# Optimization experiments

Measured on AMD Instinct MI355X. Metric: run time of the kernel, lower is better.

Reference implementation:

```python
import jax, jax.numpy as jnp
import numpy as np

LRELU = 0.2
BN_EPS = 1e-5
SN_EPS = 1e-12


def _spectral_norm(w, u):
    # One power iteration (torch train-mode behavior), u/v detached.
    wm = w.reshape(w.shape[0], -1)            # [out, in*kh*kw]
    u = jax.lax.stop_gradient(u)
    v = wm.T @ u
    v = v / (jnp.linalg.norm(v) + SN_EPS)
    u2 = wm @ v
    u2 = u2 / (jnp.linalg.norm(u2) + SN_EPS)
    sigma = u2 @ (wm @ v)
    return w / sigma


def _conv(x, w):
    # Conv2d kernel=4, stride=2, padding=1, no bias
    return jax.lax.conv_general_dilated(
        x, w, window_strides=(2, 2), padding=((1, 1), (1, 1)),
        dimension_numbers=("NCHW", "OIHW", "NCHW"))


def _bn(x, g, b):
    # BatchNorm2d in training mode: biased batch stats over (N,H,W)
    m = x.mean(axis=(0, 2, 3), keepdims=True)
    v = x.var(axis=(0, 2, 3), keepdims=True)
    xh = (x - m) * jax.lax.rsqrt(v + BN_EPS)
    return xh * g[None, :, None, None] + b[None, :, None, None]


def _lrelu(x):
    return jnp.where(x >= 0, x, LRELU * x)


def setup_inputs() -> dict:
    key = jax.random.key(0)
    ks = jax.random.split(key, 16)
    ndf, nc, oc, N = 64, 3, 64, 64
    chans = [(nc, ndf), (ndf, ndf * 2), (ndf * 2, ndf * 4),
             (ndf * 4, ndf * 4), (ndf * 4, ndf * 8), (ndf * 8, oc)]
    inp = {"image": jax.random.normal(ks[0], (N, nc, 128, 128), jnp.float32)}
    for i, (ci, co) in enumerate(chans):
        inp[f"w{i+1}"] = 0.02 * jax.random.normal(ks[1 + i], (co, ci, 4, 4), jnp.float32)
        inp[f"u{i+1}"] = jax.random.normal(ks[7 + i], (co,), jnp.float32)
    for i, c in enumerate([ndf * 2, ndf * 4, ndf * 4, ndf * 8]):
        inp[f"g{i+1}"] = jnp.ones((c,), jnp.float32)
        inp[f"b{i+1}"] = jnp.zeros((c,), jnp.float32)
    A, B, C = oc * 2 * 2, oc, ndf  # 256, 64, 64
    stddev = 1.0 / A
    inp["T"] = jax.random.uniform(ks[13], (A, B, C), jnp.float32,
                                  minval=stddev, maxval=1.0)
    return inp


def reference(image, w1, w2, w3, w4, w5, w6, u1, u2, u3, u4, u5, u6,
              g1, b1, g2, b2, g3, b3, g4, b4, T):
    x = _lrelu(_conv(image, _spectral_norm(w1, u1)))
    x = _lrelu(_bn(_conv(x, _spectral_norm(w2, u2)), g1, b1))
    x = _lrelu(_bn(_conv(x, _spectral_norm(w3, u3)), g2, b2))
    x = _lrelu(_bn(_conv(x, _spectral_norm(w4, u4)), g3, b3))
    x = _lrelu(_bn(_conv(x, _spectral_norm(w5, u5)), g4, b4))
    x = _conv(x, _spectral_norm(w6, u6))          # [N, 64, 2, 2]; Dropout2d(p=0) = identity
    A, Bo, C = T.shape
    flat = x.reshape(-1, A)                        # [N, 256]
    Ms = (flat @ T.reshape(A, Bo * C)).reshape(-1, Bo, C)   # [N, B, C]
    # MiniBatchDiscrimination: out[i,b] = sum_j exp(-||Ms[i,b]-Ms[j,b]||_1)
    d = jnp.abs(Ms[:, None, :, :] - Ms[None, :, :, :]).sum(-1)  # [N, N, B]
    mbd = jnp.exp(-d).sum(axis=1)                  # [N, B]
    return jnp.concatenate([flat, mbd], axis=1)    # [N, 320]
```

## Files before the change

### kernel.cpp

```cpp
#include <hip/hip_runtime.h>
#include <hip/hip_bf16.h>
#include <math.h>

#define LRELU 0.2f
#define BN_EPS 1e-5f
#define SN_EPS 1e-12f

typedef __attribute__((ext_vector_type(4))) float f32x4;
typedef __attribute__((ext_vector_type(8))) short bf16x8;
typedef __attribute__((ext_vector_type(4))) short bf16x4;

__device__ inline float bf2f(short s) {
  union { unsigned u; float f; } c; c.u = ((unsigned)(unsigned short)s) << 16; return c.f;
}
__device__ inline short f2bf(float f) {
  __hip_bfloat16 h = __float2bfloat16(f); return *(short*)&h;
}

__device__ inline int xcd_swz(int bx, int nwg) {
  int chunk = nwg >> 3;
  return (bx & 7) * chunk + (bx >> 3);
}

__device__ inline float blockReduceSum256(float v, volatile float* red) {
  #pragma unroll
  for (int o = 32; o > 0; o >>= 1) v += __shfl_down(v, o, 64);
  const int tid = threadIdx.x;
  __syncthreads();
  if ((tid & 63) == 0) red[tid >> 6] = v;
  __syncthreads();
  return red[0] + red[1] + red[2] + red[3];
}

struct SNArgs {
  const float* w[6];
  const float* u[6];
  int outc[6];
  int ink[6];
};

__global__ __launch_bounds__(256) void sn_v(SNArgs args, float* __restrict__ vpart) {
  const int l = blockIdx.z;
  const int in_k = args.ink[l], out_c = args.outc[l];
  const int tid = threadIdx.x;
  const int j = blockIdx.x * 256 + tid;
  if (blockIdx.x * 256 >= in_k) return;
  const int rows = out_c >> 3;
  const int i0 = blockIdx.y * rows;
  __shared__ float uS[64];
  if (tid < rows) uS[tid] = args.u[l][i0 + tid];
  __syncthreads();
  if (j >= in_k) return;
  const float* __restrict__ w = args.w[l] + (size_t)i0 * in_k;
  float t = 0.f;
  for (int i = 0; i < rows; ++i) t = fmaf(w[(size_t)i * in_k + j], uS[i], t);
  vpart[((size_t)(l * 8 + blockIdx.y)) * 8192 + j] = t;
}

__global__ __launch_bounds__(256) void sn_v_red(SNArgs args, const float* __restrict__ vpart,
                                                float* __restrict__ vbuf, float* __restrict__ pA) {
  const int l = blockIdx.y;
  const int in_k = args.ink[l];
  const int tid = threadIdx.x;
  const int j = blockIdx.x * 256 + tid;
  __shared__ float red[4];
  float s = 0.f;
  if (j < in_k) {
    #pragma unroll
    for (int ch = 0; ch < 8; ++ch)
      s += vpart[((size_t)(l * 8 + ch)) * 8192 + j];
    vbuf[l * 8192 + j] = s;
  }
  const float bs = blockReduceSum256((j < in_k) ? s * s : 0.f, red);
  if (tid == 0) pA[l * 32 + blockIdx.x] = bs;
}

__global__ __launch_bounds__(64) void sn_norm1(SNArgs args, const float* __restrict__ pA,
                                               float* __restrict__ rinv) {
  const int l = blockIdx.x;
  if (threadIdx.x != 0) return;
  const int nb = (args.ink[l] + 255) >> 8;
  float s = 0.f;
  for (int b = 0; b < nb; ++b) s += pA[l * 32 + b];
  rinv[l] = 1.f / (sqrtf(s) + SN_EPS);
}

__global__ __launch_bounds__(256) void sn_t2(SNArgs args, const float* __restrict__ vbuf,
                                             const float* __restrict__ rinv,
                                             float* __restrict__ pB) {
  const int l = blockIdx.y;
  const int in_k = args.ink[l], out_c = args.outc[l];
  const int lane = threadIdx.x & 63, wv = threadIdx.x >> 6;
  const int row = blockIdx.x * 4 + wv;
  __shared__ float red[4];
  float sq = 0.f;
  if (row < out_c) {
    const float* __restrict__ wr = args.w[l] + (size_t)row * in_k;
    const float* __restrict__ v = vbuf + l * 8192;
    float a0 = 0.f, a1 = 0.f, a2 = 0.f, a3 = 0.f;
    for (int j = lane * 4; j < in_k; j += 256) {
      f32x4 w4 = *(const f32x4*)(wr + j);
      f32x4 v4 = *(const f32x4*)(v + j);
      a0 = fmaf(w4[0], v4[0], a0);
      a1 = fmaf(w4[1], v4[1], a1);
      a2 = fmaf(w4[2], v4[2], a2);
      a3 = fmaf(w4[3], v4[3], a3);
    }
    float t = (a0 + a1) + (a2 + a3);
    #pragma unroll
    for (int o = 32; o > 0; o >>= 1) t += __shfl_down(t, o, 64);
    if (lane == 0) { t *= rinv[l]; sq = t * t; }
  }
  __syncthreads();
  if (lane == 0) red[wv] = sq;
  __syncthreads();
  if (threadIdx.x == 0) pB[l * 128 + blockIdx.x] = red[0] + red[1] + red[2] + red[3];
}

__global__ __launch_bounds__(64) void sn_norm2(const float* __restrict__ pB,
                                               float* __restrict__ inv_sigma) {
  const int l = blockIdx.x;
  if (threadIdx.x != 0) return;
  float s = 0.f;
  for (int b = 0; b < 128; ++b) s += pB[l * 128 + b];
  const float n2 = sqrtf(s);
  const float sigma = s / (n2 + SN_EPS);
  inv_sigma[l] = 1.f / sigma;
}

__global__ __launch_bounds__(256) void zero_pads(__hip_bfloat16* r0, __hip_bfloat16* r1) {
  int t = blockIdx.x * 256 + threadIdx.x;
  if (t < 2048) {
    r0[16777216 + t] = __float2bfloat16(0.f);
    r1[16777216 + t] = __float2bfloat16(0.f);
  }
}

struct PPArgs {
  const float* w[6];
  __hip_bfloat16* dst[6];
  int cinr[6];
  int cout[6];
  int kpad[6];
  int kreal[6];
};

__global__ __launch_bounds__(256) void prepack_all(PPArgs args, const float* __restrict__ invs) {
  const int l = blockIdx.y;
  int e = blockIdx.x * 256 + threadIdx.x;
  const int total = args.kpad[l] * args.cout[l];
  if (e >= total) return;
  const int CINR = args.cinr[l], COUT = args.cout[l], KREAL = args.kreal[l];
  int j = e & 7, lane = (e >> 3) & 63, frag = e >> 9;
  int nfrags = COUT >> 4;
  int ks = frag / nfrags, nf = frag - ks * nfrags;
  int k = ks * 32 + ((lane >> 4) << 3) + j;
  int co = (nf << 4) + (lane & 15);
  float val = 0.f;
  if (k < KREAL) {
    int khw = k / CINR, ci = k - khw * CINR;
    int kh = khw >> 2, kw = khw & 3;
    val = args.w[l][(((size_t)co * CINR + ci) * 4 + kh) * 4 + kw] * invs[l];
  }
  args.dst[l][e] = __float2bfloat16(val);
}

__global__ __launch_bounds__(256) void im2col_l1(const float* __restrict__ img,
                                                 __hip_bfloat16* __restrict__ a2) {
  int t = blockIdx.x * 256 + threadIdx.x;
  int c = t & 7;
  int m = t >> 3;
  int n = m >> 12;
  int hw = m & 4095;
  int ho = hw >> 6, wo = hw & 63;
  int ihb = 2 * ho - 1, iwb = 2 * wo - 1;
  const float* __restrict__ ib = img + (size_t)n * 49152;
  short vals[8];
  #pragma unroll
  for (int j = 0; j < 8; ++j) {
    int k = c * 8 + j;
    float val = 0.f;
    if (k < 48) {
      int khw = k / 3;
      int ci = k - khw * 3;
      int kh = khw >> 2, kw = khw & 3;
      int ih = ihb + kh, iw = iwb + kw;
      if (((unsigned)ih < 128u) & ((unsigned)iw < 128u))
        val = ib[ci * 16384 + ih * 128 + iw];
    }
    vals[j] = f2bf(val);
  }
  *(bf16x8*)(a2 + (size_t)m * 64 + c * 8) = *(bf16x8*)vals;
}

template<int CIN, int COUT, int MF, bool FUSE>
__global__ __launch_bounds__(256) void conv_mfma(
    const __hip_bfloat16* __restrict__ x,
    const __hip_bfloat16* __restrict__ wf,
    __hip_bfloat16* __restrict__ out)
{
  constexpr int CB = CIN / 32;

  const int bx = xcd_swz(blockIdx.x, gridDim.x);
  const int lane = threadIdx.x & 63;
  const int wid  = threadIdx.x >> 6;
  const int wm = wid >> 1, wn = wid & 1;
  const int mbase = bx * (MF * 32) + wm * (MF * 16);
  const int cobase = blockIdx.y * 64 + wn * 32;

  int offm[MF];
  #pragma unroll
  for (int mf = 0; mf < MF; ++mf) {
    int m = mbase + mf * 16 + (lane & 15);
    offm[mf] = m * CIN;
  }
  const int koff = (lane >> 4) << 3;
  const __hip_bfloat16* wfp = wf + ((size_t)((blockIdx.y * 4 + wn * 2) * 64 + lane)) * 8;

  f32x4 acc[MF][2];
  #pragma unroll
  for (int mf = 0; mf < MF; ++mf) {
    acc[mf][0] = (f32x4){0.f, 0.f, 0.f, 0.f};
    acc[mf][1] = (f32x4){0.f, 0.f, 0.f, 0.f};
  }

  #pragma unroll
  for (int cb = 0; cb < CB; ++cb) {
    bf16x8 a[MF], b[2];
    #pragma unroll
    for (int mf = 0; mf < MF; ++mf) a[mf] = *(const bf16x8*)(x + offm[mf] + koff + cb * 32);
    #pragma unroll
    for (int nf = 0; nf < 2; ++nf)
      b[nf] = *(const bf16x8*)(wfp + (size_t)cb * (COUT * 32) + nf * 512);
    #pragma unroll
    for (int mf = 0; mf < MF; ++mf)
      #pragma unroll
      for (int nf = 0; nf < 2; ++nf)
        acc[mf][nf] = __builtin_amdgcn_mfma_f32_16x16x32_bf16(a[mf], b[nf], acc[mf][nf], 0, 0, 0);
  }

  const int r0 = (lane >> 4) * 4;
  const int cw = cobase + (lane & 15);
  #pragma unroll
  for (int mf = 0; mf < MF; ++mf)
    #pragma unroll
    for (int nf = 0; nf < 2; ++nf)
      #pragma unroll
      for (int r = 0; r < 4; ++r) {
        float v = acc[mf][nf][r];
        if (FUSE) v = (v >= 0.f) ? v : LRELU * v;
        int m = mbase + mf * 16 + r0 + r;
        out[(size_t)m * COUT + (cw + nf * 16)] = __float2bfloat16(v);
      }
}

template<int CIN, int COUT, int HIN, int HOUT, int Z, bool SPLITK, bool BNIN>
__global__ __launch_bounds__(256) void conv_lds(
    const __hip_bfloat16* __restrict__ x,
    const __hip_bfloat16* __restrict__ wf,
    const float* __restrict__ sbp,
    __hip_bfloat16* __restrict__ outb)
{
  constexpr int WIN = HIN, WO = HOUT;
  constexpr int CB = CIN / 32;
  constexpr int KHW_PER = 16 / Z;
  constexpr int NSTEP = KHW_PER * CB;
  constexpr int PADOFF = 16777216;
  constexpr int M = 64 * HOUT * WO;

  __shared__ __hip_bfloat16 As[128 * 32];
  __shared__ __hip_bfloat16 Bs[4096];

  const int bx = xcd_swz(blockIdx.x, gridDim.x);
  const int t = threadIdx.x;
  const int lane = t & 63;
  const int wid = t >> 6;
  const int wm = wid >> 1, wn = wid & 1;
  const int mbase = bx * 128;
  const int nbase = blockIdx.y * 128;
  const int khw0 = blockIdx.z * KHW_PER;

  const int sr0 = t >> 2;
  const int sl  = t & 3;
  const int wchunk = sl ^ ((sr0 >> 1) & 3);
  int rowbase[2], ihbs[2], iwbs[2];
  #pragma unroll
  for (int i = 0; i < 2; ++i) {
    int m = mbase + sr0 + i * 64;
    int n = m / (HOUT * WO);
    int hw = m - n * (HOUT * WO);
    int ho = hw / WO, wo = hw - ho * WO;
    ihbs[i] = 2 * ho - 1;
    iwbs[i] = 2 * wo - 1;
    rowbase[i] = ((n * HIN + ihbs[i]) * WIN + iwbs[i]) * CIN;
  }
  const size_t bslab0 = (size_t)(nbase >> 4) * 512 + (size_t)t * 8;

  f32x4 acc[4][4];
  #pragma unroll
  for (int mf = 0; mf < 4; ++mf)
    #pragma unroll
    for (int nf = 0; nf < 4; ++nf) acc[mf][nf] = (f32x4){0.f, 0.f, 0.f, 0.f};

  bf16x8 ra0, ra1, rb0, rb1;
  f32x4 sc0, sc1, of0, of1;
  bool v0 = true, v1 = true;
  auto load_step = [&](int ks) {
    const int khw = khw0 + ks / CB;
    const int cb = ks % CB;
    const int kh = khw >> 2, kw = khw & 3;
    const int kbyteoff = cb * 32 + sl * 8;
    {
      int ih = ihbs[0] + kh, iw = iwbs[0] + kw;
      v0 = ((unsigned)ih < (unsigned)HIN) & ((unsigned)iw < (unsigned)WIN);
      int off = v0 ? (rowbase[0] + (kh * WIN + kw) * CIN + kbyteoff) : PADOFF;
      ra0 = *(const bf16x8*)(x + off);
    }
    {
      int ih = ihbs[1] + kh, iw = iwbs[1] + kw;
      v1 = ((unsigned)ih < (unsigned)HIN) & ((unsigned)iw < (unsigned)WIN);
      int off = v1 ? (rowbase[1] + (kh * WIN + kw) * CIN + kbyteoff) : PADOFF;
      ra1 = *(const bf16x8*)(x + off);
    }
    const size_t kg = (size_t)khw * CB + cb;
    const size_t bo = kg * (COUT * 32) + bslab0;
    rb0 = *(const bf16x8*)(wf + bo);
    rb1 = *(const bf16x8*)(wf + bo + 2048);
    if (BNIN) {
      const int cbv = cb * 32 + sl * 8;
      sc0 = *(const f32x4*)(sbp + cbv);
      sc1 = *(const f32x4*)(sbp + cbv + 4);
      of0 = *(const f32x4*)(sbp + CIN + cbv);
      of1 = *(const f32x4*)(sbp + CIN + cbv + 4);
    }
  };

  load_step(0);
  for (int ks = 0; ks < NSTEP; ++ks) {
    __syncthreads();
    bf16x8 wa0 = ra0, wa1 = ra1;
    if (BNIN) {
      #pragma unroll
      for (int j = 0; j < 8; ++j) {
        float sc = (j < 4) ? sc0[j] : sc1[j - 4];
        float of = (j < 4) ? of0[j] : of1[j - 4];
        float f0 = fmaf(bf2f(wa0[j]), sc, of);
        f0 = fmaxf(f0, LRELU * f0);
        wa0[j] = v0 ? f2bf(f0) : (short)0;
        float f1 = fmaf(bf2f(wa1[j]), sc, of);
        f1 = fmaxf(f1, LRELU * f1);
        wa1[j] = v1 ? f2bf(f1) : (short)0;
      }
    }
    *(bf16x8*)(&As[sr0 * 32 + wchunk * 8]) = wa0;
    *(bf16x8*)(&As[(sr0 + 64) * 32 + wchunk * 8]) = wa1;
    *(bf16x8*)(&Bs[t * 8]) = rb0;
    *(bf16x8*)(&Bs[2048 + t * 8]) = rb1;
    __syncthreads();
    if (ks + 1 < NSTEP) load_step(ks + 1);
    bf16x8 af[4], bfr[4];
    #pragma unroll
    for (int mf = 0; mf < 4; ++mf) {
      const int ra = wm * 64 + mf * 16 + (lane & 15);
      const int rc = (lane >> 4) ^ ((ra >> 1) & 3);
      af[mf] = *(const bf16x8*)(&As[ra * 32 + rc * 8]);
    }
    #pragma unroll
    for (int nf = 0; nf < 4; ++nf)
      bfr[nf] = *(const bf16x8*)(&Bs[(wn * 4 + nf) * 512 + lane * 8]);
    #pragma unroll
    for (int mf = 0; mf < 4; ++mf)
      #pragma unroll
      for (int nf = 0; nf < 4; ++nf)
        acc[mf][nf] = __builtin_amdgcn_mfma_f32_16x16x32_bf16(af[mf], bfr[nf], acc[mf][nf], 0, 0, 0);
  }

  const int r0w = (lane >> 4) * 4;
  const int cw = nbase + wn * 64 + (lane & 15);
  #pragma unroll
  for (int mf = 0; mf < 4; ++mf)
    #pragma unroll
    for (int nf = 0; nf < 4; ++nf)
      #pragma unroll
      for (int r = 0; r < 4; ++r) {
        const int m = mbase + wm * 64 + mf * 16 + r0w + r;
        const int co = cw + nf * 16;
        if (SPLITK)
          outb[(size_t)blockIdx.z * M * COUT + (size_t)m * COUT + co] = __float2bfloat16(acc[mf][nf][r]);
        else
          outb[(size_t)m * COUT + co] = __float2bfloat16(acc[mf][nf][r]);
      }
}

template<int CIN, int COUT, int HIN, int HOUT, int Z, bool SPLITK, bool BNIN, bool BF16P>
__global__ __launch_bounds__(256) void conv_mfma4(
    const __hip_bfloat16* __restrict__ x,
    const __hip_bfloat16* __restrict__ wf,
    const float* __restrict__ sbp,
    __hip_bfloat16* __restrict__ outb, float* __restrict__ outp)
{
  constexpr int WIN = HIN, WO = HOUT;
  constexpr int CB = CIN / 32;
  constexpr int KHW_PER = 16 / Z;
  constexpr int PADOFF = 16777216;
  constexpr int M = 64 * HOUT * WO;

  const int bx = xcd_swz(blockIdx.x, gridDim.x);
  const int lane = threadIdx.x & 63;
  const int wid  = threadIdx.x >> 6;
  const int wm = wid >> 1, wn = wid & 1;
  const int mbase = bx * 128 + wm * 64;
  const int nbase = blockIdx.y * 128 + wn * 64;
  const int khw0 = blockIdx.z * KHW_PER;

  int offm[4], ihb[4], iwb[4];
  #pragma unroll
  for (int mf = 0; mf < 4; ++mf) {
    int m = mbase + mf * 16 + (lane & 15);
    int n = m / (HOUT * WO);
    int hw = m - n * (HOUT * WO);
    int ho = hw / WO, wo = hw - ho * WO;
    ihb[mf] = 2 * ho - 1;
    iwb[mf] = 2 * wo - 1;
    offm[mf] = ((n * HIN + ihb[mf]) * WIN + iwb[mf]) * CIN;
  }
  const int koff = (lane >> 4) << 3;
  const __hip_bfloat16* wfp = wf + ((size_t)((nbase >> 4) * 64 + lane)) * 8;

  f32x4 acc[4][4];
  #pragma unroll
  for (int mf = 0; mf < 4; ++mf)
    #pragma unroll
    for (int nf = 0; nf < 4; ++nf) acc[mf][nf] = (f32x4){0.f, 0.f, 0.f, 0.f};

  #pragma unroll
  for (int cb = 0; cb < CB; ++cb) {
    f32x4 s0, s1, o0, o1;
    if (BNIN) {
      const int cbase = cb * 32 + koff;
      s0 = *(const f32x4*)(sbp + cbase);
      s1 = *(const f32x4*)(sbp + cbase + 4);
      o0 = *(const f32x4*)(sbp + CIN + cbase);
      o1 = *(const f32x4*)(sbp + CIN + cbase + 4);
    }
    #pragma unroll
    for (int ki = 0; ki < KHW_PER; ++ki) {
      const int khw = khw0 + ki;
      const int kh = khw >> 2, kw = khw & 3;
      bf16x8 a[4], b[4];
      bool vm[4];
      #pragma unroll
      for (int mf = 0; mf < 4; ++mf) {
        int ih = ihb[mf] + kh, iw = iwb[mf] + kw;
        vm[mf] = ((unsigned)ih < (unsigned)HIN) & ((unsigned)iw < (unsigned)WIN);
        int off = vm[mf] ? (offm[mf] + (kh * WIN + kw) * CIN + koff + cb * 32)
                         : (PADOFF + koff + cb * 32);
        a[mf] = *(const bf16x8*)(x + off);
      }
      const size_t ks = (size_t)khw * CB + cb;
      #pragma unroll
      for (int nf = 0; nf < 4; ++nf)
        b[nf] = *(const bf16x8*)(wfp + ks * (COUT * 32) + nf * 512);
      if (BNIN) {
        #pragma unroll
        for (int mf = 0; mf < 4; ++mf) {
          bf16x8 tt = a[mf];
          #pragma unroll
          for (int j = 0; j < 8; ++j) {
            float fv = bf2f(tt[j]);
            float sc = (j < 4) ? s0[j] : s1[j - 4];
            float of = (j < 4) ? o0[j] : o1[j - 4];
            fv = fmaf(fv, sc, of);
            fv = fmaxf(fv, LRELU * fv);
            tt[j] = vm[mf] ? f2bf(fv) : (short)0;
          }
          a[mf] = tt;
        }
      }
      #pragma unroll
      for (int mf = 0; mf < 4; ++mf)
        #pragma unroll
        for (int nf = 0; nf < 4; ++nf)
          acc[mf][nf] = __builtin_amdgcn_mfma_f32_16x16x32_bf16(a[mf], b[nf], acc[mf][nf], 0, 0, 0);
    }
  }

  const int r0 = (lane >> 4) * 4;
  const int cw = nbase + (lane & 15);
  #pragma unroll
  for (int mf = 0; mf < 4; ++mf)
    #pragma unroll
    for (int nf = 0; nf < 4; ++nf)
      #pragma unroll
      for (int r = 0; r < 4; ++r) {
        const int m = mbase + mf * 16 + r0 + r;
        const int co = cw + nf * 16;
        if (SPLITK) {
          if (BF16P)
            outb[(size_t)blockIdx.z * M * COUT + (size_t)m * COUT + co] = __float2bfloat16(acc[mf][nf][r]);
          else
            outp[(size_t)blockIdx.z * M * COUT + (size_t)m * COUT + co] = acc[mf][nf][r];
        } else {
          outb[(size_t)m * COUT + co] = __float2bfloat16(acc[mf][nf][r]);
        }
      }
}

template<int Z, int MCHUNKS, bool BF16P>
__global__ __launch_bounds__(256) void sk_bn_fuse(const float* __restrict__ partf,
                                                  const __hip_bfloat16* __restrict__ partb,
                                                  __hip_bfloat16* __restrict__ xo,
                                                  float* __restrict__ statp, int M, int C) {
  const int chunk = blockIdx.x;
  const int c0 = blockIdx.y * 64 + (threadIdx.x & 7) * 8;
  const int mrow = threadIdx.x >> 3;
  const int rows = M / MCHUNKS;
  const size_t MC = (size_t)M * C;
  float s[8], s2[8];
  #pragma unroll
  for (int j = 0; j < 8; ++j) { s[j] = 0.f; s2[j] = 0.f; }
  for (int mi = mrow; mi < rows; mi += 32) {
    const int m = chunk * rows + mi;
    const size_t base = (size_t)m * C + c0;
    float av[8];
    if (BF16P) {
      bf16x8 v0 = *(const bf16x8*)(partb + base);
      #pragma unroll
      for (int j = 0; j < 8; ++j) av[j] = bf2f(v0[j]);
      #pragma unroll
      for (int z = 1; z < Z; ++z) {
        bf16x8 vz = *(const bf16x8*)(partb + (size_t)z * MC + base);
        #pragma unroll
        for (int j = 0; j < 8; ++j) av[j] += bf2f(vz[j]);
      }
    } else {
      f32x4 a = *(const f32x4*)(partf + base);
      f32x4 b = *(const f32x4*)(partf + base + 4);
      #pragma unroll
      for (int z = 1; z < Z; ++z) {
        a += *(const f32x4*)(partf + (size_t)z * MC + base);
        b += *(const f32x4*)(partf + (size_t)z * MC + base + 4);
      }
      #pragma unroll
      for (int j = 0; j < 4; ++j) { av[j] = a[j]; av[4 + j] = b[j]; }
    }
    bf16x8 o;
    #pragma unroll
    for (int j = 0; j < 8; ++j) {
      o[j] = f2bf(av[j]);
      s[j] += av[j];
      s2[j] = fmaf(av[j], av[j], s2[j]);
    }
    *(bf16x8*)(xo + base) = o;
  }
  __shared__ float ls[8][256], ls2[8][256];
  const int t = threadIdx.x;
  #pragma unroll
  for (int j = 0; j < 8; ++j) { ls[j][t] = s[j]; ls2[j][t] = s2[j]; }
  __syncthreads();
  #pragma unroll
  for (int off = 16; off >= 1; off >>= 1) {
    if (mrow < off) {
      #pragma unroll
      for (int j = 0; j < 8; ++j) {
        ls[j][t]  += ls[j][t + off * 8];
        ls2[j][t] += ls2[j][t + off * 8];
      }
    }
    __syncthreads();
  }
  if (t < 8) {
    #pragma unroll
    for (int j = 0; j < 8; ++j) {
      statp[(size_t)chunk * C + c0 + j] = ls[j][t];
      statp[(size_t)(MCHUNKS + chunk) * C + c0 + j] = ls2[j][t];
    }
  }
}

__global__ __launch_bounds__(256) void conv_l6_mfma(
    const __hip_bfloat16* __restrict__ x,
    const __hip_bfloat16* __restrict__ wf,
    float* __restrict__ x6, float* __restrict__ out)
{
  constexpr int CIN = 512, COUT = 64, HIN = 4;
  constexpr int CB = CIN / 32;
  constexpr int PADOFF = 16777216;

  const int lane = threadIdx.x & 63;
  const int wid  = threadIdx.x >> 6;
  const int wm = wid >> 1, wn = wid & 1;
  const int mbase = blockIdx.x * 32 + wm * 16;

  int m0 = mbase + (lane & 15);
  int n = m0 >> 2;
  int hw = m0 & 3;
  int ho = hw >> 1, wo = hw & 1;
  int ihb = 2 * ho - 1;
  int iwb = 2 * wo - 1;
  int offm = ((n * HIN + ihb) * HIN + iwb) * CIN;

  const int koff = (lane >> 4) << 3;
  const __hip_bfloat16* wfp = wf + ((size_t)((wn * 2) * 64 + lane)) * 8;

  f32x4 acc[2];
  acc[0] = (f32x4){0.f, 0.f, 0.f, 0.f};
  acc[1] = (f32x4){0.f, 0.f, 0.f, 0.f};

  #pragma unroll
  for (int khw = 0; khw < 16; ++khw) {
    const int kh = khw >> 2, kw = khw & 3;
    const int ih = ihb + kh, iw = iwb + kw;
    const bool v = ((unsigned)ih < (unsigned)HIN) & ((unsigned)iw < (unsigned)HIN);
    const int off = v ? (offm + (kh * HIN + kw) * CIN + koff) : (PADOFF + koff);
    const __hip_bfloat16* ap = x + off;
    #pragma unroll
    for (int cb = 0; cb < CB; ++cb) {
      const int ks = khw * CB + cb;
      bf16x8 a = *(const bf16x8*)(ap + cb * 32);
      bf16x8 b0 = *(const bf16x8*)(wfp + (size_t)ks * (COUT * 32));
      bf16x8 b1 = *(const bf16x8*)(wfp + (size_t)ks * (COUT * 32) + 512);
      acc[0] = __builtin_amdgcn_mfma_f32_16x16x32_bf16(a, b0, acc[0], 0, 0, 0);
      acc[1] = __builtin_amdgcn_mfma_f32_16x16x32_bf16(a, b1, acc[1], 0, 0, 0);
    }
  }

  const int r0 = (lane >> 4) * 4;
  const int cw = wn * 32 + (lane & 15);
  #pragma unroll
  for (int nf = 0; nf < 2; ++nf)
    #pragma unroll
    for (int r = 0; r < 4; ++r) {
      int m = mbase + r0 + r;
      int nn = m >> 2, p = m & 3;
      float v = acc[nf][r];
      x6[(size_t)nn * 256 + (cw + nf * 16) * 4 + p] = v;
      out[(size_t)nn * 320 + (cw + nf * 16) * 4 + p] = v;
    }
}

template<int MCHUNKS>
__global__ __launch_bounds__(256) void bn_stats_a(const __hip_bfloat16* __restrict__ x,
                                                  float* __restrict__ part, int M, int C) {
  const int chunk = blockIdx.x;
  const int c0 = blockIdx.y * 64 + (threadIdx.x & 7) * 8;
  const int mrow = threadIdx.x >> 3;
  const int rows = M / MCHUNKS;
  float s[8], s2[8];
  #pragma unroll
  for (int j = 0; j < 8; ++j) { s[j] = 0.f; s2[j] = 0.f; }
  for (int mi = mrow; mi < rows; mi += 32) {
    const int m = chunk * rows + mi;
    bf16x8 v = *(const bf16x8*)(x + (size_t)m * C + c0);
    #pragma unroll
    for (int j = 0; j < 8; ++j) {
      float f = bf2f(v[j]);
      s[j] += f;
      s2[j] = fmaf(f, f, s2[j]);
    }
  }
  __shared__ float ls[8][256], ls2[8][256];
  const int t = threadIdx.x;
  #pragma unroll
  for (int j = 0; j < 8; ++j) { ls[j][t] = s[j]; ls2[j][t] = s2[j]; }
  __syncthreads();
  #pragma unroll
  for (int off = 16; off >= 1; off >>= 1) {
    if (mrow < off) {
      #pragma unroll
      for (int j = 0; j < 8; ++j) {
        ls[j][t]  += ls[j][t + off * 8];
        ls2[j][t] += ls2[j][t + off * 8];
      }
    }
    __syncthreads();
  }
  if (t < 8) {
    #pragma unroll
    for (int j = 0; j < 8; ++j) {
      part[(size_t)chunk * C + c0 + j] = ls[j][t];
      part[(size_t)(MCHUNKS + chunk) * C + c0 + j] = ls2[j][t];
    }
  }
}

template<int MCHUNKS>
__global__ __launch_bounds__(64) void bn_stats_b(const float* __restrict__ part,
                                                 const float* __restrict__ g,
                                                 const float* __restrict__ b,
                                                 float* __restrict__ sb, int M, int C) {
  int c = blockIdx.x * 64 + threadIdx.x;
  float s = 0.f, s2 = 0.f;
  for (int ch = 0; ch < MCHUNKS; ++ch) {
    s  += part[(size_t)ch * C + c];
    s2 += part[(size_t)(MCHUNKS + ch) * C + c];
  }
  float invM = 1.f / (float)M;
  float mean = s * invM;
  float var = s2 * invM - mean * mean;
  float scale = g[c] * rsqrtf(var + BN_EPS);
  sb[c] = scale;
  sb[C + c] = b[c] - mean * scale;
}

__global__ __launch_bounds__(256) void bn_apply(__hip_bfloat16* __restrict__ x,
                                                const float* __restrict__ sb,
                                                int C, int nvec) {
  int idx = blockIdx.x * 256 + threadIdx.x;
  if (idx >= nvec) return;
  size_t e = (size_t)idx * 8;
  int c0 = (int)(e % (size_t)C);
  bf16x8 v = *(bf16x8*)(x + e);
  bf16x8 o;
  #pragma unroll
  for (int j = 0; j < 8; ++j) {
    int c = c0 + j;
    float f = bf2f(v[j]);
    f = fmaf(f, sb[c], sb[C + c]);
    f = (f >= 0.f) ? f : LRELU * f;
    o[j] = f2bf(f);
  }
  *(bf16x8*)(x + e) = o;
}

__global__ __launch_bounds__(256) void ms_kernel(const float* __restrict__ x6,
                                                 const float* __restrict__ T,
                                                 float* __restrict__ Ms) {
  const int cb = blockIdx.x;
  const int nb = blockIdx.y;
  const int c  = threadIdx.x & 63;
  const int ns = threadIdx.x >> 6;
  __shared__ float fsh[16][256];
  for (int t = threadIdx.x; t < 4096; t += 256) {
    int n = t >> 8, a = t & 255;
    fsh[n][a] = x6[(size_t)(nb * 16 + n) * 256 + a];
  }
  __syncthreads();
  const int col = cb * 64 + c;
  float acc0 = 0.f, acc1 = 0.f, acc2 = 0.f, acc3 = 0.f;
  #pragma unroll 8
  for (int a = 0; a < 256; ++a) {
    float tv = T[(size_t)a * 4096 + col];
    acc0 = fmaf(fsh[ns * 4 + 0][a], tv, acc0);
    acc1 = fmaf(fsh[ns * 4 + 1][a], tv, acc1);
    acc2 = fmaf(fsh[ns * 4 + 2][a], tv, acc2);
    acc3 = fmaf(fsh[ns * 4 + 3][a], tv, acc3);
  }
  const int nbase = nb * 16 + ns * 4;
  Ms[(size_t)(nbase + 0) * 4096 + col] = acc0;
  Ms[(size_t)(nbase + 1) * 4096 + col] = acc1;
  Ms[(size_t)(nbase + 2) * 4096 + col] = acc2;
  Ms[(size_t)(nbase + 3) * 4096 + col] = acc3;
}

__global__ __launch_bounds__(256) void mbd_kernel(const float* __restrict__ Ms,
                                                  float* __restrict__ out) {
  const int b  = blockIdx.x;
  const int ib = blockIdx.y;
  const int tid = threadIdx.x;
  __shared__ float Mb[64][65];
  for (int idx = tid; idx < 4096; idx += 256) {
    const int i = idx >> 6, cc = idx & 63;
    Mb[i][cc] = Ms[(size_t)i * 4096 + b * 64 + cc];
  }
  __syncthreads();
  const int i  = ib * 16 + (tid >> 4);
  const int jg = tid & 15;
  float ssum = 0.f;
  for (int j = jg; j < 64; j += 16) {
    float d = 0.f;
    #pragma unroll
    for (int cc = 0; cc < 64; ++cc) d += fabsf(Mb[i][cc] - Mb[j][cc]);
    ssum += expf(-d);
  }
  ssum += __shfl_xor(ssum, 1, 64);
  ssum += __shfl_xor(ssum, 2, 64);
  ssum += __shfl_xor(ssum, 4, 64);
  ssum += __shfl_xor(ssum, 8, 64);
  if (jg == 0) out[(size_t)i * 320 + 256 + b] = ssum;
}

extern "C" void kernel_launch(void* const* d_in, const int* in_sizes, int n_in,
                              void* d_out, int out_size, void* d_ws, size_t ws_size,
                              hipStream_t stream) {
  const float* image = (const float*)d_in[0];
  const float* W[6] = {(const float*)d_in[1], (const float*)d_in[3], (const float*)d_in[5],
                       (const float*)d_in[7], (const float*)d_in[9], (const float*)d_in[11]};
  const float* U[6] = {(const float*)d_in[2], (const float*)d_in[4], (const float*)d_in[6],
                       (const float*)d_in[8], (const float*)d_in[10], (const float*)d_in[12]};
  const float* G[4] = {(const float*)d_in[13], (const float*)d_in[15],
                       (const float*)d_in[17], (const float*)d_in[19]};
  const float* Bb[4] = {(const float*)d_in[14], (const float*)d_in[16],
                        (const float*)d_in[18], (const float*)d_in[20]};
  const float* T = (const float*)d_in[21];
  float* out = (float*)d_out;

  float* f = (float*)d_ws;
  float* inv_sigma = f;
  float* part      = f + 1024;
  float* x6        = f + 1024 + 65536 + 1024;
  float* Ms        = f + 1024 + 65536 + 1024 + 16384;
  float* vbuf      = f + 360448;
  float* pA        = f + 360448 + 49152;
  float* pB        = pA + 256;
  float* rinv      = pB + 768;
  float* sbL[4];
  for (int i = 0; i < 4; ++i) sbL[i] = f + 412672 + i * 2048;
  __hip_bfloat16* bfb = (__hip_bfloat16*)(f + 524288);
  const size_t REGION = 16777216 + 2048;
  __hip_bfloat16* region0 = bfb;
  __hip_bfloat16* region1 = region0 + REGION;
  __hip_bfloat16* wf1 = region1 + REGION;
  __hip_bfloat16* wf2 = wf1 + 4096;
  __hip_bfloat16* wf3 = wf2 + 131072;
  __hip_bfloat16* wf4 = wf3 + 524288;
  __hip_bfloat16* wf5 = wf4 + 1048576;
  __hip_bfloat16* wf6 = wf5 + 2097152;
  float* skpart = (float*)(wf6 + 524288);
  __hip_bfloat16* skpartb = (__hip_bfloat16*)skpart;
  float* vpart  = skpart + 8388608;

  __hip_bfloat16* a2col = region0;
  __hip_bfloat16* x1 = region1;
  __hip_bfloat16* x2 = region0;
  __hip_bfloat16* x3 = region1;
  __hip_bfloat16* x4 = region0;
  __hip_bfloat16* x5 = region1;

  zero_pads<<<8, 256, 0, stream>>>(region0, region1);

  SNArgs sa;
  const int outc[6] = {64, 128, 256, 256, 512, 64};
  const int ink[6]  = {48, 1024, 2048, 4096, 4096, 8192};
  for (int l = 0; l < 6; ++l) { sa.w[l] = W[l]; sa.u[l] = U[l]; sa.outc[l] = outc[l]; sa.ink[l] = ink[l]; }

  sn_v<<<dim3(32, 8, 6), 256, 0, stream>>>(sa, vpart);
  sn_v_red<<<dim3(32, 6), 256, 0, stream>>>(sa, vpart, vbuf, pA);
  sn_norm1<<<6, 64, 0, stream>>>(sa, pA, rinv);
  sn_t2<<<dim3(128, 6), 256, 0, stream>>>(sa, vbuf, rinv, pB);
  sn_norm2<<<6, 64, 0, stream>>>(pB, inv_sigma);

  PPArgs pa;
  __hip_bfloat16* wfp_[6] = {wf1, wf2, wf3, wf4, wf5, wf6};
  const int cinr_[6]  = {3, 64, 128, 256, 256, 512};
  const int kpad_[6]  = {64, 1024, 2048, 4096, 4096, 8192};
  const int kreal_[6] = {48, 1024, 2048, 4096, 4096, 8192};
  for (int l = 0; l < 6; ++l) {
    pa.w[l] = W[l]; pa.dst[l] = wfp_[l]; pa.cinr[l] = cinr_[l];
    pa.cout[l] = outc[l]; pa.kpad[l] = kpad_[l]; pa.kreal[l] = kreal_[l];
  }
  prepack_all<<<dim3(8192, 6), 256, 0, stream>>>(pa, inv_sigma);

  im2col_l1<<<8192, 256, 0, stream>>>(image, a2col);

  conv_mfma<64, 64, 4, true><<<dim3(2048, 1), 256, 0, stream>>>(a2col, wf1, x1);

  conv_lds<64, 128, 64, 32, 1, false, false><<<dim3(512, 1, 1), 256, 0, stream>>>(x1, wf2, nullptr, x2);
  bn_stats_a<256><<<dim3(256, 2), 256, 0, stream>>>(x2, part, 65536, 128);
  bn_stats_b<256><<<2, 64, 0, stream>>>(part, G[0], Bb[0], sbL[0], 65536, 128);

  conv_lds<128, 256, 32, 16, 2, true, true><<<dim3(128, 2, 2), 256, 0, stream>>>(x2, wf3, sbL[0], skpartb);
  sk_bn_fuse<2, 128, true><<<dim3(128, 4), 256, 0, stream>>>(nullptr, skpartb, x3, part, 16384, 256);
  bn_stats_b<128><<<4, 64, 0, stream>>>(part, G[1], Bb[1], sbL[1], 16384, 256);

  conv_lds<256, 256, 16, 8, 8, true, true><<<dim3(32, 2, 8), 256, 0, stream>>>(x3, wf4, sbL[1], skpartb);
  sk_bn_fuse<8, 128, true><<<dim3(128, 4), 256, 0, stream>>>(nullptr, skpartb, x4, part, 4096, 256);
  bn_stats_b<128><<<4, 64, 0, stream>>>(part, G[2], Bb[2], sbL[2], 4096, 256);

  conv_mfma4<256, 512, 8, 4, 16, true, true, true><<<dim3(8, 4, 16), 256, 0, stream>>>(x4, wf5, sbL[2], skpartb, nullptr);
  sk_bn_fuse<16, 32, true><<<dim3(32, 8), 256, 0, stream>>>(nullptr, skpartb, x5, part, 1024, 512);
  bn_stats_b<32><<<8, 64, 0, stream>>>(part, G[3], Bb[3], sbL[3], 1024, 512);

  bn_apply<<<256, 256, 0, stream>>>(x5, sbL[3], 512, 65536);
  conv_l6_mfma<<<8, 256, 0, stream>>>(x5, wf6, x6, out);

  ms_kernel<<<dim3(64, 4), 256, 0, stream>>>(x6, T, Ms);
  mbd_kernel<<<dim3(64, 4), 256, 0, stream>>>(Ms, out);
}
```

Before: 334.9 us.

## Double-buffer conv LDS tiles and load weights directly to LDS

Result: slower. 345.1 us (+3.0%).

```diff
diff --git a/kernel.cpp b/kernel.cpp
--- a/kernel.cpp
+++ b/kernel.cpp
@@ -15,6 +15,12 @@
 }
 __device__ inline short f2bf(float f) {
   __hip_bfloat16 h = __float2bfloat16(f); return *(short*)&h;
+}
+
+__device__ __forceinline__ void gld_lds16(const void* g, void* l) {
+  __builtin_amdgcn_global_load_lds(
+      (const __attribute__((address_space(1))) void*)g,
+      (__attribute__((address_space(3))) void*)l, 16, 0, 0);
 }
 
 __device__ inline int xcd_swz(int bx, int nwg) {
@@ -268,8 +274,8 @@
   constexpr int PADOFF = 16777216;
   constexpr int M = 64 * HOUT * WO;
 
-  __shared__ __hip_bfloat16 As[128 * 32];
-  __shared__ __hip_bfloat16 Bs[4096];
+  __shared__ __hip_bfloat16 As[2][4096];
+  __shared__ __hip_bfloat16 Bs[2][4096];
 
   const int bx = xcd_swz(blockIdx.x, gridDim.x);
   const int t = threadIdx.x;
@@ -302,10 +308,32 @@
     #pragma unroll
     for (int nf = 0; nf < 4; ++nf) acc[mf][nf] = (f32x4){0.f, 0.f, 0.f, 0.f};
 
-  bf16x8 ra0, ra1, rb0, rb1;
+  auto issueB = [&](int ks, int buf) {
+    const int khw = khw0 + ks / CB;
+    const int cb = ks % CB;
+    const size_t kg = (size_t)khw * CB + cb;
+    const size_t bo = kg * (COUT * 32) + bslab0;
+    gld_lds16(wf + bo,        &Bs[buf][wid * 512]);
+    gld_lds16(wf + bo + 2048, &Bs[buf][2048 + wid * 512]);
+  };
+  auto issueA = [&](int ks, int buf) {
+    const int khw = khw0 + ks / CB;
+    const int cb = ks % CB;
+    const int kh = khw >> 2, kw = khw & 3;
+    const int kb = cb * 32 + sl * 8;
+    int ih0 = ihbs[0] + kh, iw0 = iwbs[0] + kw;
+    int off0 = (((unsigned)ih0 < (unsigned)HIN) & ((unsigned)iw0 < (unsigned)WIN))
+               ? (rowbase[0] + (kh * WIN + kw) * CIN + kb) : PADOFF;
+    gld_lds16(x + off0, &As[buf][wid * 512]);
+    int ih1 = ihbs[1] + kh, iw1 = iwbs[1] + kw;
+    int off1 = (((unsigned)ih1 < (unsigned)HIN) & ((unsigned)iw1 < (unsigned)WIN))
+               ? (rowbase[1] + (kh * WIN + kw) * CIN + kb) : PADOFF;
+    gld_lds16(x + off1, &As[buf][2048 + wid * 512]);
+  };
+  bf16x8 ra0, ra1;
   f32x4 sc0, sc1, of0, of1;
   bool v0 = true, v1 = true;
-  auto load_step = [&](int ks) {
+  auto loadA = [&](int ks) {
     const int khw = khw0 + ks / CB;
     const int cb = ks % CB;
     const int kh = khw >> 2, kw = khw & 3;
@@ -322,24 +350,20 @@
       int off = v1 ? (rowbase[1] + (kh * WIN + kw) * CIN + kbyteoff) : PADOFF;
       ra1 = *(const bf16x8*)(x + off);
     }
-    const size_t kg = (size_t)khw * CB + cb;
-    const size_t bo = kg * (COUT * 32) + bslab0;
-    rb0 = *(const bf16x8*)(wf + bo);
-    rb1 = *(const bf16x8*)(wf + bo + 2048);
+    const int cbv = cb * 32 + sl * 8;
+    sc0 = *(const f32x4*)(sbp + cbv);
+    sc1 = *(const f32x4*)(sbp + cbv + 4);
+    of0 = *(const f32x4*)(sbp + CIN + cbv);
+    of1 = *(const f32x4*)(sbp + CIN + cbv + 4);
+  };
+
+  if (BNIN) loadA(0); else issueA(0, 0);
+  issueB(0, 0);
+
+  for (int ks = 0; ks < NSTEP; ++ks) {
+    const int cur = ks & 1;
     if (BNIN) {
-      const int cbv = cb * 32 + sl * 8;
-      sc0 = *(const f32x4*)(sbp + cbv);
-      sc1 = *(const f32x4*)(sbp + cbv + 4);
-      of0 = *(const f32x4*)(sbp + CIN + cbv);
-      of1 = *(const f32x4*)(sbp + CIN + cbv + 4);
-    }
-  };
-
-  load_step(0);
-  for (int ks = 0; ks < NSTEP; ++ks) {
-    __syncthreads();
-    bf16x8 wa0 = ra0, wa1 = ra1;
-    if (BNIN) {
+      bf16x8 wa0 = ra0, wa1 = ra1;
       #pragma unroll
       for (int j = 0; j < 8; ++j) {
         float sc = (j < 4) ? sc0[j] : sc1[j - 4];
@@ -351,23 +375,25 @@
         f1 = fmaxf(f1, LRELU * f1);
         wa1[j] = v1 ? f2bf(f1) : (short)0;
       }
-    }
-    *(bf16x8*)(&As[sr0 * 32 + wchunk * 8]) = wa0;
-    *(bf16x8*)(&As[(sr0 + 64) * 32 + wchunk * 8]) = wa1;
-    *(bf16x8*)(&Bs[t * 8]) = rb0;
-    *(bf16x8*)(&Bs[2048 + t * 8]) = rb1;
+      *(bf16x8*)(&As[cur][sr0 * 32 + wchunk * 8]) = wa0;
+      *(bf16x8*)(&As[cur][(sr0 + 64) * 32 + wchunk * 8]) = wa1;
+    }
     __syncthreads();
-    if (ks + 1 < NSTEP) load_step(ks + 1);
+    if (ks + 1 < NSTEP) {
+      issueB(ks + 1, cur ^ 1);
+      if (BNIN) loadA(ks + 1);
+      else      issueA(ks + 1, cur ^ 1);
+    }
     bf16x8 af[4], bfr[4];
     #pragma unroll
     for (int mf = 0; mf < 4; ++mf) {
       const int ra = wm * 64 + mf * 16 + (lane & 15);
-      const int rc = (lane >> 4) ^ ((ra >> 1) & 3);
-      af[mf] = *(const bf16x8*)(&As[ra * 32 + rc * 8]);
+      const int rc = BNIN ? ((lane >> 4) ^ ((ra >> 1) & 3)) : (lane >> 4);
+      af[mf] = *(const bf16x8*)(&As[cur][ra * 32 + rc * 8]);
     }
     #pragma unroll
     for (int nf = 0; nf < 4; ++nf)
-      bfr[nf] = *(const bf16x8*)(&Bs[(wn * 4 + nf) * 512 + lane * 8]);
+      bfr[nf] = *(const bf16x8*)(&Bs[cur][(wn * 4 + nf) * 512 + lane * 8]);
     #pragma unroll
     for (int mf = 0; mf < 4; ++mf)
       #pragma unroll
```
